# Kernel tuning notes

Hardware: AMD Instinct MI355X
Metric: run time of the kernel (lower is better)

The kernel has to match this reference:

```python
import jax, jax.numpy as jnp
import numpy as np

DIM = 64

def conv2d_g2(x, w, b):
    # 3x3 conv, padding=1, groups=2, NCHW
    y = jax.lax.conv_general_dilated(x, w, (1, 1), [(1, 1), (1, 1)],
                                     dimension_numbers=('NCHW', 'OIHW', 'NCHW'),
                                     feature_group_count=2)
    return y + b[None, :, None, None]

def bilinear_gather(x, py, px):
    # x: [B,C,H,W]; py,px: [B,K,H,W] float sample coords -> [B,K,H,W,C]
    B, C, H, W = x.shape
    y0 = jnp.floor(py); x0 = jnp.floor(px)
    ly = py - y0; lx = px - x0
    hy = 1.0 - ly; hx = 1.0 - lx
    b_idx = jnp.arange(B)[:, None, None, None]
    def gather(yi, xi):
        valid = (yi >= 0) & (yi < H) & (xi >= 0) & (xi < W)
        yc = jnp.clip(yi, 0, H - 1).astype(jnp.int32)
        xc = jnp.clip(xi, 0, W - 1).astype(jnp.int32)
        v = x[b_idx, :, yc, xc]  # [B,K,H,W,C]
        return v * valid[..., None].astype(x.dtype)
    return (gather(y0, x0) * (hy * hx)[..., None]
            + gather(y0, x0 + 1) * (hy * lx)[..., None]
            + gather(y0 + 1, x0) * (ly * hx)[..., None]
            + gather(y0 + 1, x0 + 1) * (ly * lx)[..., None])

def deform_dw(x, offset, w, b, k, pad, dil):
    # depthwise (groups=C, offset_groups=1) deformable conv, stride 1
    B, C, H, W = x.shape
    K = k * k
    off = offset.reshape(B, K, 2, H, W)  # torchvision layout: (dy,dx) per kernel tap
    ky = jnp.repeat(jnp.arange(k), k).astype(x.dtype)   # [K]
    kx = jnp.tile(jnp.arange(k), k).astype(x.dtype)     # [K]
    base_y = jnp.arange(H, dtype=x.dtype)[None, None, :, None] - pad + dil * ky[None, :, None, None]
    base_x = jnp.arange(W, dtype=x.dtype)[None, None, None, :] - pad + dil * kx[None, :, None, None]
    py = base_y + off[:, :, 0]  # [B,K,H,W]
    px = base_x + off[:, :, 1]
    val = bilinear_gather(x, py, px)  # [B,K,H,W,C]
    return jnp.einsum('bkhwc,ck->bchw', val, w.reshape(C, K)) + b[None, :, None, None]

def lsk_forward(x, w_off3, b_off3, w_off2, b_off2, w7, b7, w5, b5):
    B, C, H, W = x.shape
    offset3 = conv2d_g2(x, w_off3, b_off3)            # [B,98,H,W]
    out1 = deform_dw(x, offset3, w7, b7, 7, 9, 3)     # [B,C,H,W]
    offset2 = conv2d_g2(x, w_off2, b_off2)            # [B,50,H,W]
    out2 = deform_dw(out1, offset2, w5, b5, 5, 6, 3)  # [B,C,H,W]
    feats = jnp.stack([out1, out2], axis=1)           # [B,2,C,H,W]
    gap = feats.mean(axis=(3, 4), keepdims=True)      # [B,2,C,1,1]
    attn = jax.nn.softmax(gap, axis=1)
    return jnp.sum(feats * attn, axis=1)              # [B,C,H,W]

def setup_inputs() -> dict:
    key = jax.random.key(0)
    ks = jax.random.split(key, 9)
    B, C, H, W = 4, DIM, 56, 56
    return {
        'x':      jax.random.normal(ks[0], (B, C, H, W), jnp.float32),
        'w_off3': jax.random.normal(ks[1], (98, C // 2, 3, 3), jnp.float32) * 0.05,
        'b_off3': jax.random.normal(ks[2], (98,), jnp.float32) * 0.05,
        'w_off2': jax.random.normal(ks[3], (50, C // 2, 3, 3), jnp.float32) * 0.05,
        'b_off2': jax.random.normal(ks[4], (50,), jnp.float32) * 0.05,
        'w7':     jax.random.normal(ks[5], (C, 1, 7, 7), jnp.float32) * 0.1,
        'b7':     jax.random.normal(ks[6], (C,), jnp.float32) * 0.05,
        'w5':     jax.random.normal(ks[7], (C, 1, 5, 5), jnp.float32) * 0.1,
        'b5':     jax.random.normal(ks[8], (C,), jnp.float32) * 0.05,
    }

def reference(x, w_off3, b_off3, w_off2, b_off2, w7, b7, w5, b5):
    return lsk_forward(x, w_off3, b_off3, w_off2, b_off2, w7, b7, w5, b5)
```

## Files before the change

### kernel.cpp

```cpp
#include <hip/hip_runtime.h>
#include <hip/hip_fp16.h>
#include <math.h>

#define HH 56
#define WW 56
#define CC 64
#define BB 4
#define HWA (HH*WW)

typedef _Float16 half8_t __attribute__((ext_vector_type(8)));
typedef _Float16 h2_t   __attribute__((ext_vector_type(2)));
typedef float f32x4_t __attribute__((ext_vector_type(4)));

#define QSTR (57*57*64)

__global__ __launch_bounds__(256)
void k_prep(const float* __restrict__ x,
            const float* __restrict__ w3, const float* __restrict__ w2,
            const float* __restrict__ b3, const float* __restrict__ b2,
            _Float16* __restrict__ xq1, _Float16* __restrict__ xh,
            _Float16* __restrict__ Wp, float* __restrict__ bbp) {
    int blk = blockIdx.x;
    int tid = threadIdx.x;
    if (blk < BB*56) {
        __shared__ float ld[64*57];
        int b = blk / 56, y = blk % 56;
        for (int i = tid; i < 64*56; i += 256) {
            int c = i / 56, col = i % 56;
            ld[c*57 + col] = x[((size_t)b*CC + c)*HWA + y*WW + col];
        }
        __syncthreads();
        _Float16* xqb = xq1 + (size_t)b*QSTR*4;
        for (int i = tid; i < 56*64; i += 256) {
            int w = i >> 6, c = i & 63;
            _Float16 hv = (_Float16)ld[c*57 + w];
            size_t i00 = (((size_t)y*57 + w)*64 + c)*4;
            xqb[i00 + 3] = hv;
            xqb[i00 + 64*4 + 2] = hv;
            xqb[i00 + 57*64*4 + 1] = hv;
            xqb[i00 + 57*64*4 + 64*4 + 0] = hv;
        }
        _Float16* dst = xh + (((size_t)(b*2)*56 + y)*58)*32;
        for (int i = tid; i < 2*58*32; i += 256) {
            int g = i / 1856;
            int r = i % 1856;
            int col = r / 32, ic = r % 32;
            float v = 0.f;
            if (col >= 1 && col <= 56) v = ld[(g*32 + ic)*57 + col - 1];
            dst[(size_t)g*56*58*32 + r] = (_Float16)v;
        }
    } else {
        int i = (blk - BB*56)*256 + tid;
        if (i < 46080) {
            int j    = i & 7;
            int lane = (i >> 3) & 63;
            int mt   = (i >> 9) % 5;
            int kt   = (i / 2560) % 9;
            int g    = i / 23040;
            int m  = mt*16 + (lane & 15);
            int ic = (lane >> 4)*8 + j;
            int ky = kt/3, kx = kt%3;
            float v = 0.f;
            if (m < 49)      v = w3[((g*49 + m)*32 + ic)*9 + ky*3 + kx];
            else if (m < 74) v = w2[((g*25 + (m-49))*32 + ic)*9 + ky*3 + kx];
            Wp[i] = (_Float16)v;
        } else if (i < 46240) {
            int t = i - 46080; int g = t/80, m = t%80;
            float v = 0.f;
            if (m < 49)      v = b3[g*49 + m];
            else if (m < 74) v = b2[g*25 + (m-49)];
            bbp[t] = v;
        }
    }
}

__global__ __launch_bounds__(256)
void k_convmfma(const _Float16* __restrict__ xh, const _Float16* __restrict__ Wp,
                const float* __restrict__ bb,
                float* __restrict__ off3, float* __restrict__ off2) {
    __shared__ _Float16 tile[4][3*18*32];
    int blk = blockIdx.x;
    int iy = blk % 56;
    int g  = (blk / 56) & 1;
    int b  = blk / 112;
    int wv   = threadIdx.y;
    int lane = threadIdx.x;
    int n0 = wv * 16;

    const unsigned int* xs = (const unsigned int*)xh;
    unsigned int* tl = (unsigned int*)&tile[wv][0];
#pragma unroll
    for (int i = 0; i < 14; ++i) {
        int idx = i*64 + lane;
        if (idx < 864) {
            int ic2 = idx & 15;
            int seg = idx >> 4;
            int cl = seg % 18, r = seg / 18;
            int y = iy - 1 + r, col = n0 + cl;
            unsigned int v = 0;
            if (y >= 0 && y < 56 && col < 58)
                v = xs[(((size_t)(b*2+g)*56 + y)*58 + col)*16 + ic2];
            tl[idx] = v;
        }
    }
    __syncthreads();

    int nlo = lane & 15, khi = lane >> 4;
    f32x4_t acc[5];
#pragma unroll
    for (int mt = 0; mt < 5; ++mt) acc[mt] = (f32x4_t){0.f,0.f,0.f,0.f};

    const half8_t* wp8 = (const half8_t*)Wp;
#pragma unroll
    for (int kt = 0; kt < 9; ++kt) {
        int ky = kt/3, kx = kt%3;
        half8_t bfrag = *(const half8_t*)&tile[wv][((ky*18) + nlo + kx)*32 + khi*8];
#pragma unroll
        for (int mt = 0; mt < 5; ++mt) {
            half8_t afrag = wp8[(((size_t)g*9 + kt)*5 + mt)*64 + lane];
            acc[mt] = __builtin_amdgcn_mfma_f32_16x16x32_f16(afrag, bfrag, acc[mt], 0, 0, 0);
        }
    }

    int pixcol = n0 + nlo;
    if (pixcol < 56) {
        int pix = iy*WW + pixcol;
#pragma unroll
        for (int mt = 0; mt < 5; ++mt) {
#pragma unroll
            for (int r = 0; r < 4; ++r) {
                int m = mt*16 + khi*4 + r;
                if (m < 74) {
                    float val = acc[mt][r] + bb[g*80 + m];
                    if (m < 49)
                        off3[((size_t)b*98 + g*49 + m)*HWA + pix] = val;
                    else
                        off2[((size_t)b*50 + g*25 + (m-49))*HWA + pix] = val;
                }
            }
        }
    }
}

template<int K, int KS, int PAD, bool WP>
__global__ __launch_bounds__(256)
void k_deform(const uint2* __restrict__ xq, const float* __restrict__ off,
              const float* __restrict__ wg, const float* __restrict__ bias,
              float* __restrict__ out, float* __restrict__ partial,
              _Float16* __restrict__ xqo) {
    __shared__ float lw[K*65];
    __shared__ float loffs[2*K][4];
    __shared__ int4  lmeta[4][K];
    __shared__ float red[4][64];
    int tid = threadIdx.x + threadIdx.y*64;
    int blk = blockIdx.x;
    int xcd = blk & 7;
    int idx = blk >> 3;
    int b   = xcd >> 1;
    int hw0 = (xcd & 1)*(HWA/2) + idx*4;

    for (int i = tid; i < K*64; i += 256) {
        int c = i / K, t = i % K;
        lw[t*65 + c] = wg[i];
    }
    if (tid < 2*K) {
        float4 v = *(const float4*)&off[((size_t)b*2*K + tid)*HWA + hw0];
        loffs[tid][0] = v.x; loffs[tid][1] = v.y;
        loffs[tid][2] = v.z; loffs[tid][3] = v.w;
    }
    __syncthreads();
    if (tid < 4*K) {
        int p = tid / K, t = tid % K;
        int hw = hw0 + p;
        int h = hw / WW, w = hw % WW;
        int ky = t / KS, kx = t % KS;
        float py = (float)(h - PAD + 3*ky) + loffs[2*t][p];
        float px = (float)(w - PAD + 3*kx) + loffs[2*t+1][p];
        float y0f = floorf(py), x0f = floorf(px);
        float ly = py - y0f, lx = px - x0f;
        float hy = 1.f - ly, hx = 1.f - lx;
        int y0 = (int)y0f, x0 = (int)x0f;
        float s0  = (y0   >= 0 && y0   < HH) ? hy : 0.f;
        float s1  = (y0+1 >= 0 && y0+1 < HH) ? ly : 0.f;
        float wx0 = (x0   >= 0 && x0   < WW) ? hx : 0.f;
        float wx1 = (x0+1 >= 0 && x0+1 < WW) ? lx : 0.f;
        int ys = min(max(y0 + 1, 0), 56);
        int j  = min(max(x0 + 1, 0), 56);
        int4 m;
        m.x = (ys*57 + j)*64;
        m.y = 0;
        __half2 wa = __floats2half2_rn(s0*wx0, s0*wx1);
        __half2 wb = __floats2half2_rn(s1*wx0, s1*wx1);
        m.z = *(int*)&wa;
        m.w = *(int*)&wb;
        lmeta[p][t] = m;
    }
    __syncthreads();

    int yp = threadIdx.y;
    int c  = threadIdx.x;
    int hw = hw0 + yp;
    const uint2* xqb = xq + (size_t)b*QSTR;

    float acc = 0.f;
#pragma unroll 2
    for (int t = 0; t < K; ++t) {
        int4 m = lmeta[yp][t];
        uint2 q = xqb[m.x + c];
        h2_t wA = *(h2_t*)&m.z;
        h2_t wB = *(h2_t*)&m.w;
        float v = __builtin_amdgcn_fdot2(*(h2_t*)&q.x, wA, 0.f, false);
        v = __builtin_amdgcn_fdot2(*(h2_t*)&q.y, wB, v, false);
        acc = fmaf(v, lw[t*65 + c], acc);
    }
    float val = acc + bias[c];
    out[((size_t)b*HWA + hw)*CC + c] = val;

    if (WP) {
        int y = hw / WW, w = hw % WW;
        _Float16* xb = xqo + (size_t)b*QSTR*4;
        _Float16 hv = (_Float16)val;
        size_t i00 = (((size_t)y*57 + w)*64 + c)*4;
        xb[i00 + 3] = hv;
        xb[i00 + 64*4 + 2] = hv;
        xb[i00 + 57*64*4 + 1] = hv;
        xb[i00 + 57*64*4 + 64*4 + 0] = hv;
    }

    red[yp][c] = val;
    __syncthreads();
    if (yp == 0)
        partial[((size_t)b*(HWA/4) + (hw0 >> 2))*64 + c]
            = red[0][c] + red[1][c] + red[2][c] + red[3][c];
}

__global__ void k_gapA(const float* __restrict__ p1, const float* __restrict__ p2,
                       float* __restrict__ g2) {
    __shared__ float red[4][64];
    int blk = blockIdx.x;
    int chunk = blk % 14;
    int bf    = blk / 14;
    int b     = bf >> 1;
    const float* p = (bf & 1) ? p2 : p1;
    int tid = threadIdx.x;
    int c = tid & 63, s = tid >> 6;
    float sum = 0.f;
#pragma unroll
    for (int i = 0; i < 14; ++i) {
        int j = chunk*56 + s + 4*i;
        sum += p[((size_t)b*(HWA/4) + j)*64 + c];
    }
    red[s][c] = sum;
    __syncthreads();
    if (s == 0)
        g2[((size_t)bf*14 + chunk)*64 + c]
            = red[0][c] + red[1][c] + red[2][c] + red[3][c];
}

__global__ void k_combine(const float* __restrict__ o1, const float* __restrict__ o2,
                          const float* __restrict__ g2, float* __restrict__ out) {
    __shared__ float tile[64][65];
    __shared__ float gsh[2][64];
    int blk = blockIdx.x;
    int b   = blk / (HWA/64);
    int t0  = (blk % (HWA/64)) * 64;
    int tid = threadIdx.x;
    int c = tid & 63, q = tid >> 6;

    if (tid < 128) {
        int f = tid >> 6, cc = tid & 63;
        float s = 0.f;
#pragma unroll
        for (int k = 0; k < 14; ++k)
            s += g2[((size_t)(b*2+f)*14 + k)*64 + cc];
        gsh[f][cc] = s * (1.f/HWA);
    }
    __syncthreads();

    float g1v = gsh[0][c];
    float g2v = gsh[1][c];
    float m  = fmaxf(g1v, g2v);
    float e1 = expf(g1v - m), e2 = expf(g2v - m);
    float a1 = e1 / (e1 + e2), a2 = 1.f - a1;

#pragma unroll
    for (int i = 0; i < 16; ++i) {
        int p = q + 4*i;
        size_t idx = ((size_t)b*HWA + t0 + p)*CC + c;
        tile[p][c] = o1[idx]*a1 + o2[idx]*a2;
    }
    __syncthreads();
    int p2 = tid & 63;
#pragma unroll
    for (int i = 0; i < 16; ++i) {
        int c2 = q + 4*i;
        out[((size_t)b*CC + c2)*HWA + t0 + p2] = tile[p2][c2];
    }
}

extern "C" void kernel_launch(void* const* d_in, const int* in_sizes, int n_in,
                              void* d_out, int out_size, void* d_ws, size_t ws_size,
                              hipStream_t stream) {
    const float* x      = (const float*)d_in[0];
    const float* w_off3 = (const float*)d_in[1];
    const float* b_off3 = (const float*)d_in[2];
    const float* w_off2 = (const float*)d_in[3];
    const float* b_off2 = (const float*)d_in[4];
    const float* w7     = (const float*)d_in[5];
    const float* b7     = (const float*)d_in[6];
    const float* w5     = (const float*)d_in[7];
    const float* b5     = (const float*)d_in[8];
    float* out = (float*)d_out;

    float* ws    = (float*)d_ws;
    float* off3r = ws;
    float* off2r = off3r + 1229312;
    float* out1  = off2r + 627200;
    float* out2  = out1  + 802816;
    float* xq1f  = out2  + 802816;
    float* xq2f  = xq1f  + 1663488;
    float* xhf   = xq2f  + 1663488;
    float* part1 = xhf   + 415744;
    float* part2 = part1 + 200704;
    float* gpA   = part2 + 200704;
    float* wpf   = gpA   + 7168;
    float* bbp   = wpf   + 23040;
    _Float16* xq1 = (_Float16*)xq1f;
    _Float16* xq2 = (_Float16*)xq2f;
    _Float16* xh  = (_Float16*)xhf;
    _Float16* Wp  = (_Float16*)wpf;
    size_t need = (size_t)(1229312 + 627200 + 802816*2 + 1663488*2 + 415744
                           + 200704*2 + 7168 + 23040 + 160) * 4;
    if (ws_size < need) return;

    k_prep<<<BB*56 + 181, 256, 0, stream>>>(x, w_off3, w_off2, b_off3, b_off2,
                                            xq1, xh, Wp, bbp);
    k_convmfma<<<BB*2*56, dim3(64,4), 0, stream>>>(xh, Wp, bbp, off3r, off2r);
    k_deform<49,7,9,true><<<BB*(HWA/4), dim3(64,4), 0, stream>>>(
        (const uint2*)xq1, off3r, w7, b7, out1, part1, xq2);
    k_deform<25,5,6,false><<<BB*(HWA/4), dim3(64,4), 0, stream>>>(
        (const uint2*)xq2, off2r, w5, b5, out2, part2, nullptr);
    k_gapA<<<8*14, 256, 0, stream>>>(part1, part2, gpA);
    k_combine<<<BB*(HWA/64), 256, 0, stream>>>(out1, out2, gpA, out);
}
```

Baseline: 162.6 us.

## Build quad-packed fp16 tables with gather-style writes and fold validity into weights

The padded quad table (four bilinear neighbours per channel) is now built by reading two input rows and writing one packed uint2 per entry, instead of scattering four separate fp16 stores per pixel. This applies both in prep and in a new k_quado kernel that rebuilds the table from out1, replacing the fused scatter writes in the first deform kernel. Out-of-range handling becomes a single validity test on the quad index that zeroes all four weights, and the address uses byte offsets. This adds one kernel launch and an extra read of out1, and the simpler validity test drops partial-border samples differently.

Measured after the change: 180.1 us. 10.7% more time.

```diff
diff --git a/kernel.cpp b/kernel.cpp
--- a/kernel.cpp
+++ b/kernel.cpp
@@ -12,45 +12,55 @@
 typedef _Float16 h2_t   __attribute__((ext_vector_type(2)));
 typedef float f32x4_t __attribute__((ext_vector_type(4)));
 
-#define QSTR (57*57*64)
+#define QE (57*57*64)
 
 __global__ __launch_bounds__(256)
 void k_prep(const float* __restrict__ x,
             const float* __restrict__ w3, const float* __restrict__ w2,
             const float* __restrict__ b3, const float* __restrict__ b2,
-            _Float16* __restrict__ xq1, _Float16* __restrict__ xh,
+            uint2* __restrict__ xq, _Float16* __restrict__ xh,
             _Float16* __restrict__ Wp, float* __restrict__ bbp) {
     int blk = blockIdx.x;
     int tid = threadIdx.x;
-    if (blk < BB*56) {
-        __shared__ float ld[64*57];
-        int b = blk / 56, y = blk % 56;
-        for (int i = tid; i < 64*56; i += 256) {
-            int c = i / 56, col = i % 56;
-            ld[c*57 + col] = x[((size_t)b*CC + c)*HWA + y*WW + col];
+    if (blk < BB*57) {
+        __shared__ float ld[2*64*57];
+        int b = blk / 57, ys = blk % 57;
+        for (int i = tid; i < 2*64*56; i += 256) {
+            int r   = i / (64*56);
+            int rem = i % (64*56);
+            int c = rem / 56, col = rem % 56;
+            int y = ys - 1 + r;
+            float v = 0.f;
+            if (y >= 0 && y < HH)
+                v = x[((size_t)b*CC + c)*HWA + y*WW + col];
+            ld[r*(64*57) + c*57 + col] = v;
         }
         __syncthreads();
-        _Float16* xqb = xq1 + (size_t)b*QSTR*4;
-        for (int i = tid; i < 56*64; i += 256) {
-            int w = i >> 6, c = i & 63;
-            _Float16 hv = (_Float16)ld[c*57 + w];
-            size_t i00 = (((size_t)y*57 + w)*64 + c)*4;
-            xqb[i00 + 3] = hv;
-            xqb[i00 + 64*4 + 2] = hv;
-            xqb[i00 + 57*64*4 + 1] = hv;
-            xqb[i00 + 57*64*4 + 64*4 + 0] = hv;
-        }
-        _Float16* dst = xh + (((size_t)(b*2)*56 + y)*58)*32;
-        for (int i = tid; i < 2*58*32; i += 256) {
-            int g = i / 1856;
-            int r = i % 1856;
-            int col = r / 32, ic = r % 32;
-            float v = 0.f;
-            if (col >= 1 && col <= 56) v = ld[(g*32 + ic)*57 + col - 1];
-            dst[(size_t)g*56*58*32 + r] = (_Float16)v;
+        uint2* dst = xq + ((size_t)b*57 + ys)*57*64;
+        for (int i = tid; i < 57*64; i += 256) {
+            int j = i >> 6, c = i & 63;
+            float l0 = (j >= 1)  ? ld[c*57 + j - 1]           : 0.f;
+            float h0 = (j < 56)  ? ld[c*57 + j]               : 0.f;
+            float l1 = (j >= 1)  ? ld[64*57 + c*57 + j - 1]   : 0.f;
+            float h1 = (j < 56)  ? ld[64*57 + c*57 + j]       : 0.f;
+            __half2 a = __floats2half2_rn(l0, h0);
+            __half2 bq = __floats2half2_rn(l1, h1);
+            uint2 q; q.x = *(unsigned*)&a; q.y = *(unsigned*)&bq;
+            dst[(size_t)j*64 + c] = q;
+        }
+        if (ys < 56) {
+            _Float16* dsth = xh + (((size_t)(b*2)*56 + ys)*58)*32;
+            for (int i = tid; i < 2*58*32; i += 256) {
+                int g = i / 1856;
+                int r = i % 1856;
+                int col = r / 32, ic = r % 32;
+                float v = 0.f;
+                if (col >= 1 && col <= 56) v = ld[64*57 + (g*32 + ic)*57 + col - 1];
+                dsth[(size_t)g*56*58*32 + r] = (_Float16)v;
+            }
         }
     } else {
-        int i = (blk - BB*56)*256 + tid;
+        int i = (blk - BB*57)*256 + tid;
         if (i < 46080) {
             int j    = i & 7;
             int lane = (i >> 3) & 63;
@@ -142,12 +152,40 @@
     }
 }
 
-template<int K, int KS, int PAD, bool WP>
+__global__ void k_quado(const float* __restrict__ o, uint2* __restrict__ xq) {
+    __shared__ float ld[2*56*64];
+    int blk = blockIdx.x;
+    int b = blk / 57, ys = blk % 57;
+    int tid = threadIdx.x;
+    for (int i = tid; i < 2*56*64; i += 256) {
+        int r   = i / (56*64);
+        int rem = i % (56*64);
+        int y = ys - 1 + r;
+        float v = 0.f;
+        if (y >= 0 && y < HH)
+            v = o[((size_t)b*HWA + y*WW)*CC + rem];
+        ld[i] = v;
+    }
+    __syncthreads();
+    uint2* dst = xq + ((size_t)b*57 + ys)*57*64;
+    for (int i = tid; i < 57*64; i += 256) {
+        int j = i >> 6, c = i & 63;
+        float l0 = (j >= 1) ? ld[(j-1)*64 + c]           : 0.f;
+        float h0 = (j < 56) ? ld[j*64 + c]               : 0.f;
+        float l1 = (j >= 1) ? ld[56*64 + (j-1)*64 + c]   : 0.f;
+        float h1 = (j < 56) ? ld[56*64 + j*64 + c]       : 0.f;
+        __half2 a = __floats2half2_rn(l0, h0);
+        __half2 bq = __floats2half2_rn(l1, h1);
+        uint2 q; q.x = *(unsigned*)&a; q.y = *(unsigned*)&bq;
+        dst[(size_t)j*64 + c] = q;
+    }
+}
+
+template<int K, int KS, int PAD>
 __global__ __launch_bounds__(256)
 void k_deform(const uint2* __restrict__ xq, const float* __restrict__ off,
               const float* __restrict__ wg, const float* __restrict__ bias,
-              float* __restrict__ out, float* __restrict__ partial,
-              _Float16* __restrict__ xqo) {
+              float* __restrict__ out, float* __restrict__ partial) {
     __shared__ float lw[K*65];
     __shared__ float loffs[2*K][4];
     __shared__ int4  lmeta[4][K];
@@ -179,18 +217,17 @@
         float y0f = floorf(py), x0f = floorf(px);
         float ly = py - y0f, lx = px - x0f;
         float hy = 1.f - ly, hx = 1.f - lx;
-        int y0 = (int)y0f, x0 = (int)x0f;
-        float s0  = (y0   >= 0 && y0   < HH) ? hy : 0.f;
-        float s1  = (y0+1 >= 0 && y0+1 < HH) ? ly : 0.f;
-        float wx0 = (x0   >= 0 && x0   < WW) ? hx : 0.f;
-        float wx1 = (x0+1 >= 0 && x0+1 < WW) ? lx : 0.f;
-        int ys = min(max(y0 + 1, 0), 56);
-        int j  = min(max(x0 + 1, 0), 56);
+        int ys = (int)y0f + 1;
+        int j  = (int)x0f + 1;
+        bool valid = (ys >= 0) & (ys <= 56) & (j >= 0) & (j <= 56);
+        float vf = valid ? 1.f : 0.f;
+        int ysc = valid ? ys : 0;
+        int jc  = valid ? j  : 0;
         int4 m;
-        m.x = (ys*57 + j)*64;
+        m.x = (ysc*57 + jc)*512;
         m.y = 0;
-        __half2 wa = __floats2half2_rn(s0*wx0, s0*wx1);
-        __half2 wb = __floats2half2_rn(s1*wx0, s1*wx1);
+        __half2 wa = __floats2half2_rn(hy*hx*vf, hy*lx*vf);
+        __half2 wb = __floats2half2_rn(ly*hx*vf, ly*lx*vf);
         m.z = *(int*)&wa;
         m.w = *(int*)&wb;
         lmeta[p][t] = m;
@@ -200,13 +237,13 @@
     int yp = threadIdx.y;
     int c  = threadIdx.x;
     int hw = hw0 + yp;
-    const uint2* xqb = xq + (size_t)b*QSTR;
+    const char* xc = (const char*)xq + (size_t)b*QE*8 + c*8;
 
     float acc = 0.f;
 #pragma unroll 2
     for (int t = 0; t < K; ++t) {
         int4 m = lmeta[yp][t];
-        uint2 q = xqb[m.x + c];
+        uint2 q = *(const uint2*)(xc + m.x);
         h2_t wA = *(h2_t*)&m.z;
         h2_t wB = *(h2_t*)&m.w;
         float v = __builtin_amdgcn_fdot2(*(h2_t*)&q.x, wA, 0.f, false);
@@ -215,17 +252,6 @@
     }
     float val = acc + bias[c];
     out[((size_t)b*HWA + hw)*CC + c] = val;
-
-    if (WP) {
-        int y = hw / WW, w = hw % WW;
-        _Float16* xb = xqo + (size_t)b*QSTR*4;
-        _Float16 hv = (_Float16)val;
-        size_t i00 = (((size_t)y*57 + w)*64 + c)*4;
-        xb[i00 + 3] = hv;
-        xb[i00 + 64*4 + 2] = hv;
-        xb[i00 + 57*64*4 + 1] = hv;
-        xb[i00 + 57*64*4 + 64*4 + 0] = hv;
-    }
 
     red[yp][c] = val;
     __syncthreads();
@@ -312,34 +338,36 @@
     const float* b5     = (const float*)d_in[8];
     float* out = (float*)d_out;
 
+    const size_t QF = (size_t)BB*QE*2;
     float* ws    = (float*)d_ws;
     float* off3r = ws;
     float* off2r = off3r + 1229312;
     float* out1  = off2r + 627200;
     float* out2  = out1  + 802816;
     float* xq1f  = out2  + 802816;
-    float* xq2f  = xq1f  + 1663488;
-    float* xhf   = xq2f  + 1663488;
+    float* xq2f  = xq1f  + QF;
+    float* xhf   = xq2f  + QF;
     float* part1 = xhf   + 415744;
     float* part2 = part1 + 200704;
     float* gpA   = part2 + 200704;
     float* wpf   = gpA   + 7168;
     float* bbp   = wpf   + 23040;
-    _Float16* xq1 = (_Float16*)xq1f;
-    _Float16* xq2 = (_Float16*)xq2f;
+    uint2* xq1 = (uint2*)xq1f;
+    uint2* xq2 = (uint2*)xq2f;
     _Float16* xh  = (_Float16*)xhf;
     _Float16* Wp  = (_Float16*)wpf;
     size_t need = (size_t)(1229312 + 627200 + 802816*2 + 1663488*2 + 415744
                            + 200704*2 + 7168 + 23040 + 160) * 4;
     if (ws_size < need) return;
 
-    k_prep<<<BB*56 + 181, 256, 0, stream>>>(x, w_off3, w_off2, b_off3, b_off2,
+    k_prep<<<BB*57 + 181, 256, 0, stream>>>(x, w_off3, w_off2, b_off3, b_off2,
                                             xq1, xh, Wp, bbp);
     k_convmfma<<<BB*2*56, dim3(64,4), 0, stream>>>(xh, Wp, bbp, off3r, off2r);
-    k_deform<49,7,9,true><<<BB*(HWA/4), dim3(64,4), 0, stream>>>(
-        (const uint2*)xq1, off3r, w7, b7, out1, part1, xq2);
-    k_deform<25,5,6,false><<<BB*(HWA/4), dim3(64,4), 0, stream>>>(
-        (const uint2*)xq2, off2r, w5, b5, out2, part2, nullptr);
+    k_deform<49,7,9><<<BB*(HWA/4), dim3(64,4), 0, stream>>>(
+        xq1, off3r, w7, b7, out1, part1);
+    k_quado<<<BB*57, 256, 0, stream>>>(out1, xq2);
+    k_deform<25,5,6><<<BB*(HWA/4), dim3(64,4), 0, stream>>>(
+        xq2, off2r, w5, b5, out2, part2);
     k_gapA<<<8*14, 256, 0, stream>>>(part1, part2, gpA);
     k_combine<<<BB*(HWA/64), 256, 0, stream>>>(out1, out2, gpA, out);
 }
```
